# Kernel tuning notes

Measured on AMD Instinct MI355X. Metric: run time of the kernel, lower is better.

## Reference

```python
import jax, jax.numpy as jnp
import numpy as np

N, G = 10000, 200          # nodes, graphs
EL, EG = 160000, 500000    # local / global edges
S, V = 256, 64             # scalar / vector hidden dims
NA, NB = 16, 5             # atom types, bond types


def _lin(k, i, o):
    return (jax.random.normal(k, (i, o), jnp.float32) / np.sqrt(i))


def scatter_mean(vals, idx, num_segments):
    # vals: [N, ...]; idx: [N] int
    sums = jax.ops.segment_sum(vals, idx, num_segments=num_segments)
    cnt = jax.ops.segment_sum(jnp.ones((vals.shape[0],), vals.dtype), idx,
                              num_segments=num_segments)
    cnt = jnp.maximum(cnt, 1.0).reshape((-1,) + (1,) * (vals.ndim - 1))
    return sums / cnt


def calc_edge_attrs(edge_index, pos):
    src, tgt = edge_index[0], edge_index[1]
    r = pos[tgt] - pos[src]                      # [E,3]
    a = (pos[tgt] * pos[src]).sum(-1)            # [E]
    d = jnp.sqrt(jnp.clip((r ** 2).sum(-1), 1e-6))
    r_norm = r / d[:, None]
    return d, a, r_norm


def setup_inputs() -> dict:
    key = jax.random.key(0)
    ks = jax.random.split(key, 24)
    inp = {}
    inp["x"] = jax.random.normal(ks[0], (N, NA), jnp.float32)
    inp["t"] = jax.random.uniform(ks[1], (G, 1), jnp.float32)
    inp["pos"] = jax.random.normal(ks[2], (N, 3), jnp.float32)
    eil = jax.random.randint(ks[3], (2, EL), 0, N)
    eig = jax.random.randint(ks[4], (2, EG), 0, N)
    # avoid self-edges so edge distances are strictly positive (safe sqrt grads)
    eig = eig.at[1].set(jnp.where(eig[1] == eig[0], (eig[1] + 1) % N, eig[1]))
    eil = eil.at[1].set(jnp.where(eil[1] == eil[0], (eil[1] + 1) % N, eil[1]))
    inp["edge_index_local"] = eil
    inp["edge_index_global"] = eig
    inp["edge_attr_global"] = jax.random.normal(ks[5], (EG, NB), jnp.float32)
    inp["batch"] = jnp.sort(jax.random.randint(ks[6], (N,), 0, G))
    # learned parameters
    inp["W_time"], inp["b_time"] = _lin(ks[7], 1, S), jnp.zeros((S,), jnp.float32)
    inp["W_atom"], inp["b_atom"] = _lin(ks[8], NA, S), jnp.zeros((S,), jnp.float32)
    inp["W_at"], inp["b_at"] = _lin(ks[9], S, S), jnp.zeros((S,), jnp.float32)
    inp["W_shared"], inp["b_shared"] = _lin(ks[10], S, S), jnp.zeros((S,), jnp.float32)
    inp["W_b0"], inp["b_b0"] = _lin(ks[11], S + 1, S), jnp.zeros((S,), jnp.float32)
    inp["W_b1"], inp["b_b1"] = _lin(ks[12], S, 2 * NB), jnp.zeros((2 * NB,), jnp.float32)
    inp["W_coord"] = _lin(ks[13], V, 2)           # no bias
    inp["W_atoms"], inp["b_atoms"] = _lin(ks[14], S, 2 * NA), jnp.zeros((2 * NA,), jnp.float32)
    return inp


def reference(x, t, pos, edge_attr_global, W_time, b_time, W_atom, b_atom,
              W_at, b_at, W_shared, b_shared, W_b0, b_b0, W_b1, b_b1,
              W_coord, W_atoms, b_atoms,
              edge_index_local, edge_index_global, batch):
    # --- trunk: center positions, embed atoms + time ---
    pos = pos - scatter_mean(pos, batch, G)[batch]
    temb = t @ W_time + b_time                    # [G,S]
    tnode = temb[batch]                           # [N,S]
    s = x @ W_atom + b_atom
    s = (s + tnode) @ W_at + b_at                 # [N,S]
    # --- edge attrs (gather-compute pattern feeding the GNN) ---
    d_l, a_l, rn_l = calc_edge_attrs(edge_index_local, pos)
    d_g, a_g, rn_g = calc_edge_attrs(edge_index_global, pos)
    # GNN stand-in (identity on s, v, p): v initialized to zeros as in original
    v = jnp.zeros((N, 3, V), s.dtype)
    # --- prediction head ---
    s = jax.nn.silu(s @ W_shared + b_shared)
    j, i = edge_index_global[0], edge_index_global[1]
    d = jnp.sqrt(((pos[i] - pos[j]) ** 2).sum(-1, keepdims=True))  # [EG,1]
    edge = jnp.concatenate([s[i] + s[j], d], axis=-1)              # [EG,S+1]
    bonds = jax.nn.silu(edge @ W_b0 + b_b0) @ W_b1 + b_b1          # [EG,2*NB]
    bonds_pred, bonds_eps = bonds[:, :NB], bonds[:, NB:]
    coords = jnp.einsum('nkv,vo->nko', v, W_coord)                 # [N,3,2]
    coords = coords - scatter_mean(coords, batch, G)[batch]
    coords_eps0, coords_eps1 = coords[..., 0], coords[..., 1]      # [N,3]
    atoms = s @ W_atoms + b_atoms                                  # [N,2*NA]
    atoms_eps, atoms_pred = atoms[:, :NA], atoms[:, NA:]
    pos_c = pos - scatter_mean(pos, batch, G)[batch]
    coords_pred = pos_c + coords_eps1
    return (coords_pred, coords_eps0, atoms_pred, atoms_eps,
            bonds_pred, bonds_eps, d_l, rn_l, a_g, rn_g)
```

## Files before the change

kernel.cpp:

```cpp
#include <hip/hip_runtime.h>
#include <hip/hip_bf16.h>

typedef __hip_bfloat16 bf16;
typedef short bf16x8 __attribute__((ext_vector_type(8)));
typedef float f32x4 __attribute__((ext_vector_type(4)));
typedef float f32x2 __attribute__((ext_vector_type(2)));

#define N_NODES  10000
#define G_GRAPHS 200
#define EL_EDGES 160000
#define EG_EDGES 500000
#define S_DIM    256
#define APAD     264

#define BONDS_BLOCKS 15625
#define LOCAL_BLOCKS 625
#define B1ROW    280

#define WS_FLAG   0
#define WS_POSC   1024
#define WS_WD     31232
#define WS_BB1    34304
#define WS_WATOM  34560
#define WS_WTIME  38656
#define WS_BTIME  38912
#define WS_BATOM  39168
#define WS_BAT    39424
#define WS_BSH    39680
#define WS_BATOMS 39936
#define WS_T      40000
#define WS_X      40448
#define WT_AT     200448
#define WT_SH     233216
#define WT_B0     265984
#define WT_ATOMS  298752
#define WS_B1F8   302848
#define WS_H      303968
#define WS_BB0R   943968
#define WS_END_FLOATS 944224

#define CHAN(S)    ((((S) >> 6) << 6) + (((S) & 3) << 4) + (((S) & 63) >> 2))
#define CHANINV(k) ((((k) >> 6) << 6) + (((k) & 15) << 2) + (((k) >> 4) & 3))

#define O_CPRED 0
#define O_CEPS  30000
#define O_APRED 60000
#define O_AEPS  220000
#define O_BPRED 380000
#define O_BEPS  2880000
#define O_DL    5380000
#define O_RNL   5540000
#define O_AG    6020000
#define O_RNG   6520000

__device__ __forceinline__ float b2f(bf16 v) { return __bfloat162float(v); }
__device__ __forceinline__ bf16  f2b(float v) { return __float2bfloat16(v); }
__device__ __forceinline__ unsigned short bbits(float v) {
    bf16 b = f2b(v);
    return *reinterpret_cast<unsigned short*>(&b);
}
__device__ __forceinline__ float ldin(const void* p, int idx, int isf32) {
    return isf32 ? ((const float*)p)[idx] : b2f(((const bf16*)p)[idx]);
}
__device__ __forceinline__ void stout(void* out, int f32o, size_t idx, float v) {
    if (f32o) ((float*)out)[idx] = v;
    else      ((bf16*)out)[idx]  = f2b(v);
}
__device__ __forceinline__ float silu(float p) {
    return p * __builtin_amdgcn_rcpf(1.0f + __expf(-p));
}
__device__ __forceinline__ int dtype_f32(const void* tt) {
    const unsigned short* q = (const unsigned short*)tt;
    int c = 0;
#pragma unroll
    for (int z = 0; z < 32; ++z) c += (q[z] >= 0x4000) ? 1 : 0;
    return c > 0;
}

__global__ void k_prep(const void* __restrict__ x, const void* __restrict__ tt,
                       const void* __restrict__ W_time, const void* __restrict__ b_time,
                       const void* __restrict__ W_atom, const void* __restrict__ b_atom,
                       const void* __restrict__ W_at, const void* __restrict__ b_at,
                       const void* __restrict__ W_shared, const void* __restrict__ b_shared,
                       const void* __restrict__ W_b0, const void* __restrict__ b_b0,
                       const void* __restrict__ W_b1, const void* __restrict__ b_b1,
                       const void* __restrict__ W_atoms, const void* __restrict__ b_atoms,
                       float* __restrict__ ws) {
    const int t = blockIdx.x * blockDim.x + threadIdx.x;
    const int f = dtype_f32(tt);
    if (t == 0) ws[WS_FLAG] = f ? 1.0f : 0.0f;
    if (t < 65536) {
        const int k = t >> 8, n = t & 255;
        ((unsigned short*)(ws + WT_AT))[n * 256 + k] = bbits(ldin(W_at, t, f));
        ((unsigned short*)(ws + WT_SH))[n * 256 + k] = bbits(ldin(W_shared, t, f));
        ((unsigned short*)(ws + WT_B0))[n * 256 + k] = bbits(ldin(W_b0, t, f));
    }
    if (t < 160000) ws[WS_X + t] = ldin(x, t, f);
    if (t < 8192) {
        const int k = t >> 5, n = t & 31;
        ((unsigned short*)(ws + WT_ATOMS))[n * 256 + k] = bbits(ldin(W_atoms, t, f));
    }
    if (t < 4480) {
        const int n = t / B1ROW, s = t - n * B1ROW;
        float v = (n < 10 && s < 256) ? ldin(W_b1, CHAN(s) * 10 + n, f) : 0.0f;
        int enc = __builtin_amdgcn_cvt_pk_fp8_f32(v, 0.0f, 0, false);
        ((unsigned char*)(ws + WS_B1F8))[t] = (unsigned char)(enc & 0xff);
    }
    if (t < 4096) ws[WS_WATOM + t] = ldin(W_atom, t, f);
    if (t < 256) {
        ws[WS_WD + t]   = ldin(W_b0, 65536 + CHAN(t), f);
        ws[WS_BB0R + t] = ldin(b_b0, t, f);
        ws[WS_WTIME + t] = ldin(W_time, t, f);
        ws[WS_BTIME + t] = ldin(b_time, t, f);
        ws[WS_BATOM + t] = ldin(b_atom, t, f);
        ws[WS_BAT + t]   = ldin(b_at, t, f);
        ws[WS_BSH + t]   = ldin(b_shared, t, f);
    }
    if (t < 200) ws[WS_T + t] = ldin(tt, t, f);
    if (t < 32)  ws[WS_BATOMS + t] = ldin(b_atoms, t, f);
    if (t < 16)  ws[WS_BB1 + t] = (t < 10) ? ldin(b_b1, t, f) : 0.0f;
}

__global__ void k_pos(const void* __restrict__ pos, const int* __restrict__ batch,
                      float* __restrict__ ws, void* __restrict__ out) {
    const int g = blockIdx.x;
    const int f32o = ws[WS_FLAG] != 0.0f;
    __shared__ int s_lo, s_hi;
    __shared__ float wsum[4][3];
    __shared__ float mean[3];
    if (threadIdx.x == 0) {
        int lo = 0, hi = N_NODES;
        while (lo < hi) { int m = (lo + hi) >> 1; if (batch[m] < g) lo = m + 1; else hi = m; }
        s_lo = lo;
        int lo2 = lo; hi = N_NODES;
        while (lo2 < hi) { int m = (lo2 + hi) >> 1; if (batch[m] < g + 1) lo2 = m + 1; else hi = m; }
        s_hi = lo2;
    }
    __syncthreads();
    const int lo = s_lo, hi = s_hi, cnt = hi - lo;
    float sx = 0.f, sy = 0.f, sz = 0.f;
    for (int n = lo + threadIdx.x; n < hi; n += 256) {
        sx += ldin(pos, n * 3 + 0, f32o);
        sy += ldin(pos, n * 3 + 1, f32o);
        sz += ldin(pos, n * 3 + 2, f32o);
    }
#pragma unroll
    for (int off = 32; off > 0; off >>= 1) {
        sx += __shfl_down(sx, off);
        sy += __shfl_down(sy, off);
        sz += __shfl_down(sz, off);
    }
    if ((threadIdx.x & 63) == 0) {
        wsum[threadIdx.x >> 6][0] = sx;
        wsum[threadIdx.x >> 6][1] = sy;
        wsum[threadIdx.x >> 6][2] = sz;
    }
    __syncthreads();
    if (threadIdx.x == 0) {
        float inv = 1.0f / (float)max(cnt, 1);
        mean[0] = (wsum[0][0] + wsum[1][0] + wsum[2][0] + wsum[3][0]) * inv;
        mean[1] = (wsum[0][1] + wsum[1][1] + wsum[2][1] + wsum[3][1]) * inv;
        mean[2] = (wsum[0][2] + wsum[1][2] + wsum[2][2] + wsum[3][2]) * inv;
    }
    __syncthreads();
    for (int n = lo + threadIdx.x; n < hi; n += 256) {
#pragma unroll
        for (int k = 0; k < 3; ++k) {
            float p = ldin(pos, n * 3 + k, f32o) - mean[k];
            ws[WS_POSC + n * 3 + k] = p;
            stout(out, f32o, O_CPRED + n * 3 + k, p);
            stout(out, f32o, O_CEPS + n * 3 + k, 0.0f);
        }
    }
}

__global__ __launch_bounds__(256) void k_node(
    const int* __restrict__ batch, const float* __restrict__ ws,
    unsigned int* __restrict__ h_out, void* __restrict__ out) {
    __shared__ unsigned short actA[16][APAD];
    __shared__ unsigned short actB[16][APAD];
    const int tid = threadIdx.x;
    const int wave = tid >> 6, lane = tid & 63;
    const int quad = lane >> 4, l16 = lane & 15;
    const int row0 = blockIdx.x * 16;

    {
        const int r = tid >> 4;
        const int c0 = (tid & 15) * 16;
        const int g = row0 + r;
        float tb = ws[WS_T + batch[g]];
        float xr[16];
#pragma unroll
        for (int k = 0; k < 16; ++k) xr[k] = ws[WS_X + g * 16 + k];
        for (int cc = 0; cc < 16; cc += 4) {
            const int c = c0 + cc;
            float a0 = ws[WS_BATOM + c + 0] + tb * ws[WS_WTIME + c + 0] + ws[WS_BTIME + c + 0];
            float a1 = ws[WS_BATOM + c + 1] + tb * ws[WS_WTIME + c + 1] + ws[WS_BTIME + c + 1];
            float a2 = ws[WS_BATOM + c + 2] + tb * ws[WS_WTIME + c + 2] + ws[WS_BTIME + c + 2];
            float a3 = ws[WS_BATOM + c + 3] + tb * ws[WS_WTIME + c + 3] + ws[WS_BTIME + c + 3];
#pragma unroll
            for (int k = 0; k < 16; ++k) {
                float4 w4 = *(const float4*)(ws + WS_WATOM + k * S_DIM + c);
                a0 += xr[k] * w4.x; a1 += xr[k] * w4.y;
                a2 += xr[k] * w4.z; a3 += xr[k] * w4.w;
            }
            actA[r][c + 0] = bbits(a0); actA[r][c + 1] = bbits(a1);
            actA[r][c + 2] = bbits(a2); actA[r][c + 3] = bbits(a3);
        }
    }
    __syncthreads();

    const unsigned short* wt_at = (const unsigned short*)(ws + WT_AT);
    const unsigned short* wt_sh = (const unsigned short*)(ws + WT_SH);
    const unsigned short* wt_b0 = (const unsigned short*)(ws + WT_B0);
    const unsigned short* wt_am = (const unsigned short*)(ws + WT_ATOMS);
    const int n0 = wave * 64;

    {
        f32x4 acc[4] = {};
        for (int kk = 0; kk < S_DIM; kk += 32) {
            const int k = kk + quad * 8;
            bf16x8 a = *(const bf16x8*)&actA[l16][k];
#pragma unroll
            for (int nt = 0; nt < 4; ++nt) {
                bf16x8 b = *(const bf16x8*)(wt_at + (size_t)(n0 + nt * 16 + l16) * S_DIM + k);
                acc[nt] = __builtin_amdgcn_mfma_f32_16x16x32_bf16(a, b, acc[nt], 0, 0, 0);
            }
        }
#pragma unroll
        for (int nt = 0; nt < 4; ++nt) {
            const int n = n0 + nt * 16 + l16;
            const float bv = ws[WS_BAT + n];
#pragma unroll
            for (int r = 0; r < 4; ++r)
                actB[quad * 4 + r][n] = bbits(acc[nt][r] + bv);
        }
    }
    __syncthreads();

    {
        f32x4 acc[4] = {};
        for (int kk = 0; kk < S_DIM; kk += 32) {
            const int k = kk + quad * 8;
            bf16x8 a = *(const bf16x8*)&actB[l16][k];
#pragma unroll
            for (int nt = 0; nt < 4; ++nt) {
                bf16x8 b = *(const bf16x8*)(wt_sh + (size_t)(n0 + nt * 16 + l16) * S_DIM + k);
                acc[nt] = __builtin_amdgcn_mfma_f32_16x16x32_bf16(a, b, acc[nt], 0, 0, 0);
            }
        }
        __syncthreads();
#pragma unroll
        for (int nt = 0; nt < 4; ++nt) {
            const int n = n0 + nt * 16 + l16;
            const float bv = ws[WS_BSH + n];
#pragma unroll
            for (int r = 0; r < 4; ++r)
                actA[quad * 4 + r][n] = bbits(silu(acc[nt][r] + bv));
        }
    }
    __syncthreads();

    {
        f32x4 acc[4] = {};
        for (int kk = 0; kk < S_DIM; kk += 32) {
            const int k = kk + quad * 8;
            bf16x8 a = *(const bf16x8*)&actA[l16][k];
#pragma unroll
            for (int nt = 0; nt < 4; ++nt) {
                bf16x8 b = *(const bf16x8*)(wt_b0 + (size_t)(n0 + nt * 16 + l16) * S_DIM + k);
                acc[nt] = __builtin_amdgcn_mfma_f32_16x16x32_bf16(a, b, acc[nt], 0, 0, 0);
            }
        }
        float bh[4];
#pragma unroll
        for (int nt = 0; nt < 4; ++nt) bh[nt] = 0.5f * ws[WS_BB0R + n0 + nt * 16 + l16];
#pragma unroll
        for (int r = 0; r < 4; ++r) {
            const int g = row0 + quad * 4 + r;
            int w = 0;
            w = __builtin_amdgcn_cvt_pk_fp8_f32(acc[0][r] + bh[0], acc[1][r] + bh[1], w, false);
            w = __builtin_amdgcn_cvt_pk_fp8_f32(acc[2][r] + bh[2], acc[3][r] + bh[3], w, true);
            h_out[(size_t)g * 64 + wave * 16 + l16] = (unsigned int)w;
        }
    }

    if (wave < 2) {
        f32x4 acc = {};
        const int n = wave * 16 + l16;
        for (int kk = 0; kk < S_DIM; kk += 32) {
            const int k = kk + quad * 8;
            bf16x8 a = *(const bf16x8*)&actA[l16][k];
            bf16x8 b = *(const bf16x8*)(wt_am + (size_t)n * S_DIM + k);
            acc = __builtin_amdgcn_mfma_f32_16x16x32_bf16(a, b, acc, 0, 0, 0);
        }
        const float bv = ws[WS_BATOMS + n];
        const int f32o = ws[WS_FLAG] != 0.0f;
#pragma unroll
        for (int r = 0; r < 4; ++r) {
            const int g = row0 + quad * 4 + r;
            float v = acc[r] + bv;
            if (n < 16) stout(out, f32o, O_AEPS + (size_t)g * 16 + n, v);
            else        stout(out, f32o, O_APRED + (size_t)g * 16 + (n - 16), v);
        }
    }
}

__global__ __launch_bounds__(256, 7) void k_edges(const int* __restrict__ eig,
                                                  const int* __restrict__ eil,
                                                  const float* __restrict__ ws,
                                                  const unsigned char* __restrict__ h,
                                                  void* __restrict__ out) {
    __shared__ unsigned char sm[2][32][272];
    __shared__ float cwd[256];
    __shared__ long cwb1l[16 * B1ROW / 8];
    unsigned char* cwb1 = (unsigned char*)cwb1l;
    const int f32o = ws[WS_FLAG] != 0.0f;

    if (blockIdx.x >= BONDS_BLOCKS) {
        const int e = (blockIdx.x - BONDS_BLOCKS) * 256 + threadIdx.x;
        const float* posc = ws + WS_POSC;
        const int s = eil[e];
        const int t = eil[EL_EDGES + e];
        float rx = posc[t * 3 + 0] - posc[s * 3 + 0];
        float ry = posc[t * 3 + 1] - posc[s * 3 + 1];
        float rz = posc[t * 3 + 2] - posc[s * 3 + 2];
        float dsq = rx * rx + ry * ry + rz * rz;
        float d = sqrtf(fmaxf(dsq, 1e-6f));
        float inv = 1.0f / d;
        stout(out, f32o, O_DL + e, d);
        stout(out, f32o, O_RNL + (size_t)e * 3 + 0, rx * inv);
        stout(out, f32o, O_RNL + (size_t)e * 3 + 1, ry * inv);
        stout(out, f32o, O_RNL + (size_t)e * 3 + 2, rz * inv);
        return;
    }

    {
        const int t = threadIdx.x;
        cwd[t] = ws[WS_WD + t];
        const unsigned int* src = (const unsigned int*)(ws + WS_B1F8);
        unsigned int* dst = (unsigned int*)cwb1;
        for (int q = t; q < 16 * B1ROW / 4; q += 256) dst[q] = src[q];
    }

    const int wave = threadIdx.x >> 6, lane = threadIdx.x & 63;
    const int quad = lane >> 4, l16 = lane & 15;
    const int P = wave >> 1, sub = wave & 1;
    const int e0 = blockIdx.x * 32 + P * 16;

    uint4 tmp[4];
#pragma unroll
    for (int p = 0; p < 4; ++p) {
        const int r16 = p * 4 + quad;
        const int es = e0 + r16;
        const int node = sub ? eig[es] : eig[EG_EDGES + es];
        tmp[p] = *(const uint4*)(h + (size_t)node * 256 + l16 * 16);
    }
#pragma unroll
    for (int p = 0; p < 4; ++p) {
        const int row = sub * 16 + p * 4 + quad;
        *(uint4*)&sm[P][row][l16 * 16] = tmp[p];
    }

    if (sub == 0) {
        const int e = e0 + l16;
        const int j = eig[e];
        const int i = eig[EG_EDGES + e];
        const float* posc = ws + WS_POSC;
        float pix = posc[i * 3 + 0], piy = posc[i * 3 + 1], piz = posc[i * 3 + 2];
        float pjx = posc[j * 3 + 0], pjy = posc[j * 3 + 1], pjz = posc[j * 3 + 2];
        float rx = pix - pjx, ry = piy - pjy, rz = piz - pjz;
        float dsq = rx * rx + ry * ry + rz * rz;
        if (quad == 0) {
            float ag = pix * pjx + piy * pjy + piz * pjz;
            float inv = 1.0f / sqrtf(fmaxf(dsq, 1e-6f));
            stout(out, f32o, O_AG + e, ag);
            stout(out, f32o, O_RNG + (size_t)e * 3 + 0, rx * inv);
            stout(out, f32o, O_RNG + (size_t)e * 3 + 1, ry * inv);
            stout(out, f32o, O_RNG + (size_t)e * 3 + 2, rz * inv);
            *(float*)&sm[P][l16][256] = sqrtf(dsq);
        }
    }
    __syncthreads();

    const float d = *(const float*)&sm[P][l16][256];
    const unsigned char* cw = cwb1 + (size_t)l16 * B1ROW;

    const int kbase = sub * 128;
    f32x4 acc = {};
#pragma unroll
    for (int t = 0; t < 4; ++t) {
        const int k = kbase + t * 32 + quad * 8;
        uint2 uaw = *(const uint2*)&sm[P][l16][k];
        uint2 ubw = *(const uint2*)&sm[P][16 + l16][k];
        float4 wA = *(const float4*)(cwd + k);
        float4 wB = *(const float4*)(cwd + k + 4);
        f32x2 a01 = __builtin_amdgcn_cvt_pk_f32_fp8((int)uaw.x, false);
        f32x2 a23 = __builtin_amdgcn_cvt_pk_f32_fp8((int)uaw.x, true);
        f32x2 a45 = __builtin_amdgcn_cvt_pk_f32_fp8((int)uaw.y, false);
        f32x2 a67 = __builtin_amdgcn_cvt_pk_f32_fp8((int)uaw.y, true);
        f32x2 b01 = __builtin_amdgcn_cvt_pk_f32_fp8((int)ubw.x, false);
        f32x2 b23 = __builtin_amdgcn_cvt_pk_f32_fp8((int)ubw.x, true);
        f32x2 b45 = __builtin_amdgcn_cvt_pk_f32_fp8((int)ubw.y, false);
        f32x2 b67 = __builtin_amdgcn_cvt_pk_f32_fp8((int)ubw.y, true);
        float u0 = silu(fmaf(d, wA.x, a01.x + b01.x));
        float u1 = silu(fmaf(d, wA.y, a01.y + b01.y));
        float u2 = silu(fmaf(d, wA.z, a23.x + b23.x));
        float u3 = silu(fmaf(d, wA.w, a23.y + b23.y));
        float u4 = silu(fmaf(d, wB.x, a45.x + b45.x));
        float u5 = silu(fmaf(d, wB.y, a45.y + b45.y));
        float u6 = silu(fmaf(d, wB.z, a67.x + b67.x));
        float u7 = silu(fmaf(d, wB.w, a67.y + b67.y));
        int lo = __builtin_amdgcn_cvt_pk_fp8_f32(u0, u1, 0, false);
        lo = __builtin_amdgcn_cvt_pk_fp8_f32(u2, u3, lo, true);
        int hi = __builtin_amdgcn_cvt_pk_fp8_f32(u4, u5, 0, false);
        hi = __builtin_amdgcn_cvt_pk_fp8_f32(u6, u7, hi, true);
        long a64 = (long)(((unsigned long)(unsigned int)hi << 32) | (unsigned int)lo);
        long b64 = *(const long*)(cw + k);
        acc = __builtin_amdgcn_mfma_f32_16x16x32_fp8_fp8(a64, b64, acc, 0, 0, 0);
    }

    __syncthreads();
    f32x4* sc = (f32x4*)&sm[P][0][0];
    if (sub == 1) sc[lane] = acc;
    __syncthreads();
    if (sub == 0 && l16 < 10) {
        f32x4 o = sc[lane];
        const float bv = ws[WS_BB1 + l16];
#pragma unroll
        for (int r = 0; r < 4; ++r) {
            const int er = e0 + quad * 4 + r;
            float v = acc[r] + o[r] + bv;
            if (l16 < 5) stout(out, f32o, O_BPRED + (size_t)er * 5 + l16, v);
            else         stout(out, f32o, O_BEPS + (size_t)er * 5 + (l16 - 5), v);
        }
    }
}

extern "C" void kernel_launch(void* const* d_in, const int* in_sizes, int n_in,
                              void* d_out, int out_size, void* d_ws, size_t ws_size,
                              hipStream_t stream) {
    const void* x        = d_in[0];
    const void* t        = d_in[1];
    const void* pos      = d_in[2];
    const int*  eil      = (const int*)d_in[3];
    const int*  eig      = (const int*)d_in[4];
    const int*  batch    = (const int*)d_in[6];
    const void* W_time   = d_in[7];
    const void* b_time   = d_in[8];
    const void* W_atom   = d_in[9];
    const void* b_atom   = d_in[10];
    const void* W_at     = d_in[11];
    const void* b_at     = d_in[12];
    const void* W_shared = d_in[13];
    const void* b_shared = d_in[14];
    const void* W_b0     = d_in[15];
    const void* b_b0     = d_in[16];
    const void* W_b1     = d_in[17];
    const void* b_b1     = d_in[18];
    const void* W_atoms  = d_in[20];
    const void* b_atoms  = d_in[21];
    (void)in_sizes; (void)n_in; (void)out_size;

    const size_t NEED = (size_t)WS_END_FLOATS * sizeof(float);
    if (ws_size < NEED) return;

    float* ws = (float*)d_ws;
    unsigned int* hbuf = (unsigned int*)(ws + WS_H);

    k_prep<<<640, 256, 0, stream>>>(x, t, W_time, b_time, W_atom, b_atom,
                                    W_at, b_at, W_shared, b_shared, W_b0, b_b0,
                                    W_b1, b_b1, W_atoms, b_atoms, ws);
    k_pos<<<G_GRAPHS, 256, 0, stream>>>(pos, batch, ws, d_out);
    k_node<<<N_NODES / 16, 256, 0, stream>>>(batch, ws, hbuf, d_out);
    k_edges<<<BONDS_BLOCKS + LOCAL_BLOCKS, 256, 0, stream>>>(
        eig, eil, ws, (const unsigned char*)hbuf, d_out);
}
```

Before: 222.7 us.

## Process 32 node rows per block in k_node to reuse weight fragments

The node MLP kernel now handles 32 rows per block instead of 16. Each weight B-fragment loaded from global memory feeds two MFMAs, which halves weight traffic per row, and the grid drops from 625 to 313 blocks. The two activation buffers are merged into a single shared buffer, with an extra barrier added so a layer's outputs are not written while other waves are still reading its inputs. Bounds checks cover the partial last block. The node kernel is small next to the edge kernel, so any end-to-end effect is likely minor, and fewer blocks means less parallelism on this step.

```diff
diff --git a/kernel.cpp b/kernel.cpp
--- a/kernel.cpp
+++ b/kernel.cpp
@@ -13,6 +13,8 @@
 #define S_DIM    256
 #define APAD     264
 
+#define NODE_M       32
+#define NODE_BLOCKS  313
 #define BONDS_BLOCKS 15625
 #define LOCAL_BLOCKS 625
 #define B1ROW    280
@@ -177,35 +179,41 @@
 __global__ __launch_bounds__(256) void k_node(
     const int* __restrict__ batch, const float* __restrict__ ws,
     unsigned int* __restrict__ h_out, void* __restrict__ out) {
-    __shared__ unsigned short actA[16][APAD];
-    __shared__ unsigned short actB[16][APAD];
+    __shared__ unsigned short act[NODE_M][APAD];
     const int tid = threadIdx.x;
     const int wave = tid >> 6, lane = tid & 63;
     const int quad = lane >> 4, l16 = lane & 15;
-    const int row0 = blockIdx.x * 16;
+    const int row0 = blockIdx.x * NODE_M;
 
     {
-        const int r = tid >> 4;
-        const int c0 = (tid & 15) * 16;
+        const int r = tid >> 3;
+        const int c0 = (tid & 7) * 32;
         const int g = row0 + r;
-        float tb = ws[WS_T + batch[g]];
-        float xr[16];
-#pragma unroll
-        for (int k = 0; k < 16; ++k) xr[k] = ws[WS_X + g * 16 + k];
-        for (int cc = 0; cc < 16; cc += 4) {
-            const int c = c0 + cc;
-            float a0 = ws[WS_BATOM + c + 0] + tb * ws[WS_WTIME + c + 0] + ws[WS_BTIME + c + 0];
-            float a1 = ws[WS_BATOM + c + 1] + tb * ws[WS_WTIME + c + 1] + ws[WS_BTIME + c + 1];
-            float a2 = ws[WS_BATOM + c + 2] + tb * ws[WS_WTIME + c + 2] + ws[WS_BTIME + c + 2];
-            float a3 = ws[WS_BATOM + c + 3] + tb * ws[WS_WTIME + c + 3] + ws[WS_BTIME + c + 3];
-#pragma unroll
-            for (int k = 0; k < 16; ++k) {
-                float4 w4 = *(const float4*)(ws + WS_WATOM + k * S_DIM + c);
-                a0 += xr[k] * w4.x; a1 += xr[k] * w4.y;
-                a2 += xr[k] * w4.z; a3 += xr[k] * w4.w;
-            }
-            actA[r][c + 0] = bbits(a0); actA[r][c + 1] = bbits(a1);
-            actA[r][c + 2] = bbits(a2); actA[r][c + 3] = bbits(a3);
+        if (g < N_NODES) {
+            float tb = ws[WS_T + batch[g]];
+            float xr[16];
+#pragma unroll
+            for (int k = 0; k < 16; ++k) xr[k] = ws[WS_X + g * 16 + k];
+            for (int cc = 0; cc < 32; cc += 4) {
+                const int c = c0 + cc;
+                float a0 = ws[WS_BATOM + c + 0] + tb * ws[WS_WTIME + c + 0] + ws[WS_BTIME + c + 0];
+                float a1 = ws[WS_BATOM + c + 1] + tb * ws[WS_WTIME + c + 1] + ws[WS_BTIME + c + 1];
+                float a2 = ws[WS_BATOM + c + 2] + tb * ws[WS_WTIME + c + 2] + ws[WS_BTIME + c + 2];
+                float a3 = ws[WS_BATOM + c + 3] + tb * ws[WS_WTIME + c + 3] + ws[WS_BTIME + c + 3];
+#pragma unroll
+                for (int k = 0; k < 16; ++k) {
+                    float4 w4 = *(const float4*)(ws + WS_WATOM + k * S_DIM + c);
+                    a0 += xr[k] * w4.x; a1 += xr[k] * w4.y;
+                    a2 += xr[k] * w4.z; a3 += xr[k] * w4.w;
+                }
+                act[r][c + 0] = bbits(a0); act[r][c + 1] = bbits(a1);
+                act[r][c + 2] = bbits(a2); act[r][c + 3] = bbits(a3);
+            }
+        } else {
+            for (int cc = 0; cc < 32; cc += 4) {
+                const int c = c0 + cc;
+                act[r][c] = 0; act[r][c + 1] = 0; act[r][c + 2] = 0; act[r][c + 3] = 0;
+            }
         }
     }
     __syncthreads();
@@ -217,36 +225,43 @@
     const int n0 = wave * 64;
 
     {
-        f32x4 acc[4] = {};
+        f32x4 acc[2][4] = {};
         for (int kk = 0; kk < S_DIM; kk += 32) {
             const int k = kk + quad * 8;
-            bf16x8 a = *(const bf16x8*)&actA[l16][k];
+            bf16x8 a0 = *(const bf16x8*)&act[l16][k];
+            bf16x8 a1 = *(const bf16x8*)&act[16 + l16][k];
 #pragma unroll
             for (int nt = 0; nt < 4; ++nt) {
                 bf16x8 b = *(const bf16x8*)(wt_at + (size_t)(n0 + nt * 16 + l16) * S_DIM + k);
-                acc[nt] = __builtin_amdgcn_mfma_f32_16x16x32_bf16(a, b, acc[nt], 0, 0, 0);
-            }
-        }
+                acc[0][nt] = __builtin_amdgcn_mfma_f32_16x16x32_bf16(a0, b, acc[0][nt], 0, 0, 0);
+                acc[1][nt] = __builtin_amdgcn_mfma_f32_16x16x32_bf16(a1, b, acc[1][nt], 0, 0, 0);
+            }
+        }
+        __syncthreads();
 #pragma unroll
         for (int nt = 0; nt < 4; ++nt) {
             const int n = n0 + nt * 16 + l16;
             const float bv = ws[WS_BAT + n];
 #pragma unroll
-            for (int r = 0; r < 4; ++r)
-                actB[quad * 4 + r][n] = bbits(acc[nt][r] + bv);
+            for (int mt = 0; mt < 2; ++mt)
+#pragma unroll
+                for (int r = 0; r < 4; ++r)
+                    act[mt * 16 + quad * 4 + r][n] = bbits(acc[mt][nt][r] + bv);
         }
     }
     __syncthreads();
 
     {
-        f32x4 acc[4] = {};
+        f32x4 acc[2][4] = {};
         for (int kk = 0; kk < S_DIM; kk += 32) {
             const int k = kk + quad * 8;
-            bf16x8 a = *(const bf16x8*)&actB[l16][k];
+            bf16x8 a0 = *(const bf16x8*)&act[l16][k];
+            bf16x8 a1 = *(const bf16x8*)&act[16 + l16][k];
 #pragma unroll
             for (int nt = 0; nt < 4; ++nt) {
                 bf16x8 b = *(const bf16x8*)(wt_sh + (size_t)(n0 + nt * 16 + l16) * S_DIM + k);
-                acc[nt] = __builtin_amdgcn_mfma_f32_16x16x32_bf16(a, b, acc[nt], 0, 0, 0);
+                acc[0][nt] = __builtin_amdgcn_mfma_f32_16x16x32_bf16(a0, b, acc[0][nt], 0, 0, 0);
+                acc[1][nt] = __builtin_amdgcn_mfma_f32_16x16x32_bf16(a1, b, acc[1][nt], 0, 0, 0);
             }
         }
         __syncthreads();
@@ -255,42 +270,51 @@
             const int n = n0 + nt * 16 + l16;
             const float bv = ws[WS_BSH + n];
 #pragma unroll
-            for (int r = 0; r < 4; ++r)
-                actA[quad * 4 + r][n] = bbits(silu(acc[nt][r] + bv));
+            for (int mt = 0; mt < 2; ++mt)
+#pragma unroll
+                for (int r = 0; r < 4; ++r)
+                    act[mt * 16 + quad * 4 + r][n] = bbits(silu(acc[mt][nt][r] + bv));
         }
     }
     __syncthreads();
 
     {
-        f32x4 acc[4] = {};
+        f32x4 acc[2][4] = {};
         for (int kk = 0; kk < S_DIM; kk += 32) {
             const int k = kk + quad * 8;
-            bf16x8 a = *(const bf16x8*)&actA[l16][k];
+            bf16x8 a0 = *(const bf16x8*)&act[l16][k];
+            bf16x8 a1 = *(const bf16x8*)&act[16 + l16][k];
 #pragma unroll
             for (int nt = 0; nt < 4; ++nt) {
                 bf16x8 b = *(const bf16x8*)(wt_b0 + (size_t)(n0 + nt * 16 + l16) * S_DIM + k);
-                acc[nt] = __builtin_amdgcn_mfma_f32_16x16x32_bf16(a, b, acc[nt], 0, 0, 0);
+                acc[0][nt] = __builtin_amdgcn_mfma_f32_16x16x32_bf16(a0, b, acc[0][nt], 0, 0, 0);
+                acc[1][nt] = __builtin_amdgcn_mfma_f32_16x16x32_bf16(a1, b, acc[1][nt], 0, 0, 0);
             }
         }
         float bh[4];
 #pragma unroll
         for (int nt = 0; nt < 4; ++nt) bh[nt] = 0.5f * ws[WS_BB0R + n0 + nt * 16 + l16];
 #pragma unroll
-        for (int r = 0; r < 4; ++r) {
-            const int g = row0 + quad * 4 + r;
-            int w = 0;
-            w = __builtin_amdgcn_cvt_pk_fp8_f32(acc[0][r] + bh[0], acc[1][r] + bh[1], w, false);
-            w = __builtin_amdgcn_cvt_pk_fp8_f32(acc[2][r] + bh[2], acc[3][r] + bh[3], w, true);
-            h_out[(size_t)g * 64 + wave * 16 + l16] = (unsigned int)w;
-        }
-    }
-
-    if (wave < 2) {
+        for (int mt = 0; mt < 2; ++mt)
+#pragma unroll
+            for (int r = 0; r < 4; ++r) {
+                const int g = row0 + mt * 16 + quad * 4 + r;
+                if (g < N_NODES) {
+                    int w = 0;
+                    w = __builtin_amdgcn_cvt_pk_fp8_f32(acc[mt][0][r] + bh[0], acc[mt][1][r] + bh[1], w, false);
+                    w = __builtin_amdgcn_cvt_pk_fp8_f32(acc[mt][2][r] + bh[2], acc[mt][3][r] + bh[3], w, true);
+                    h_out[(size_t)g * 64 + wave * 16 + l16] = (unsigned int)w;
+                }
+            }
+    }
+
+    {
         f32x4 acc = {};
-        const int n = wave * 16 + l16;
+        const int mt = wave >> 1;
+        const int n = (wave & 1) * 16 + l16;
         for (int kk = 0; kk < S_DIM; kk += 32) {
             const int k = kk + quad * 8;
-            bf16x8 a = *(const bf16x8*)&actA[l16][k];
+            bf16x8 a = *(const bf16x8*)&act[mt * 16 + l16][k];
             bf16x8 b = *(const bf16x8*)(wt_am + (size_t)n * S_DIM + k);
             acc = __builtin_amdgcn_mfma_f32_16x16x32_bf16(a, b, acc, 0, 0, 0);
         }
@@ -298,10 +322,12 @@
         const int f32o = ws[WS_FLAG] != 0.0f;
 #pragma unroll
         for (int r = 0; r < 4; ++r) {
-            const int g = row0 + quad * 4 + r;
-            float v = acc[r] + bv;
-            if (n < 16) stout(out, f32o, O_AEPS + (size_t)g * 16 + n, v);
-            else        stout(out, f32o, O_APRED + (size_t)g * 16 + (n - 16), v);
+            const int g = row0 + mt * 16 + quad * 4 + r;
+            if (g < N_NODES) {
+                float v = acc[r] + bv;
+                if (n < 16) stout(out, f32o, O_AEPS + (size_t)g * 16 + n, v);
+                else        stout(out, f32o, O_APRED + (size_t)g * 16 + (n - 16), v);
+            }
         }
     }
 }
@@ -472,7 +498,7 @@
                                     W_at, b_at, W_shared, b_shared, W_b0, b_b0,
                                     W_b1, b_b1, W_atoms, b_atoms, ws);
     k_pos<<<G_GRAPHS, 256, 0, stream>>>(pos, batch, ws, d_out);
-    k_node<<<N_NODES / 16, 256, 0, stream>>>(batch, ws, hbuf, d_out);
+    k_node<<<NODE_BLOCKS, 256, 0, stream>>>(batch, ws, hbuf, d_out);
     k_edges<<<BONDS_BLOCKS + LOCAL_BLOCKS, 256, 0, stream>>>(
         eig, eil, ws, (const unsigned char*)hbuf, d_out);
 }
```

After: 234.3 us. +5.2%, slower.

## Fold atom, W_at and shared linear layers into one matrix; merge prep kernels

Applied to the files above, without the earlier changes.

With no nonlinearity between them, the atom embedding, time embedding, W_at and W_shared layers are algebraically folded into a single 16x256 matrix plus a time vector and bias. One dedicated block of a merged pre-kernel computes this fold in fp32. The per-node kernel then does a small 16-wide product followed by silu, dropping two 256x256 MFMA GEMMs per node tile and the conversion of those weights. The old prep and pos-centering kernels become one launch, and x is read directly instead of being copied. The cost is a serial single-block fold, whose latency may sit on the critical path before the node kernel starts.

```diff
diff --git a/kernel.cpp b/kernel.cpp
--- a/kernel.cpp
+++ b/kernel.cpp
@@ -13,34 +13,33 @@
 #define S_DIM    256
 #define APAD     264
 
+#define NODE_BLOCKS  625
 #define BONDS_BLOCKS 15625
 #define LOCAL_BLOCKS 625
 #define B1ROW    280
 
+#define PRE_CONV 256
+#define PRE_FOLD 256
+#define PRE_POS  257
+#define PRE_BLOCKS 457
+
 #define WS_FLAG   0
 #define WS_POSC   1024
 #define WS_WD     31232
-#define WS_BB1    34304
-#define WS_WATOM  34560
-#define WS_WTIME  38656
-#define WS_BTIME  38912
-#define WS_BATOM  39168
-#define WS_BAT    39424
-#define WS_BSH    39680
-#define WS_BATOMS 39936
-#define WS_T      40000
-#define WS_X      40448
-#define WT_AT     200448
-#define WT_SH     233216
-#define WT_B0     265984
-#define WT_ATOMS  298752
-#define WS_B1F8   302848
-#define WS_H      303968
-#define WS_BB0R   943968
-#define WS_END_FLOATS 944224
+#define WS_BB1    31744
+#define WS_WX     31760
+#define WS_WT2    35856
+#define WS_B2     36112
+#define WS_BATOMS 36368
+#define WS_T      36400
+#define WS_BB0R   36608
+#define WT_B0     36864
+#define WT_ATOMS  69632
+#define WS_B1F8   73728
+#define WS_H      74848
+#define WS_END_FLOATS 714848
 
 #define CHAN(S)    ((((S) >> 6) << 6) + (((S) & 3) << 4) + (((S) & 63) >> 2))
-#define CHANINV(k) ((((k) >> 6) << 6) + (((k) & 15) << 2) + (((k) >> 4) & 3))
 
 #define O_CPRED 0
 #define O_CEPS  30000
@@ -77,108 +76,132 @@
     return c > 0;
 }
 
-__global__ void k_prep(const void* __restrict__ x, const void* __restrict__ tt,
-                       const void* __restrict__ W_time, const void* __restrict__ b_time,
-                       const void* __restrict__ W_atom, const void* __restrict__ b_atom,
-                       const void* __restrict__ W_at, const void* __restrict__ b_at,
-                       const void* __restrict__ W_shared, const void* __restrict__ b_shared,
-                       const void* __restrict__ W_b0, const void* __restrict__ b_b0,
-                       const void* __restrict__ W_b1, const void* __restrict__ b_b1,
-                       const void* __restrict__ W_atoms, const void* __restrict__ b_atoms,
-                       float* __restrict__ ws) {
-    const int t = blockIdx.x * blockDim.x + threadIdx.x;
-    const int f = dtype_f32(tt);
-    if (t == 0) ws[WS_FLAG] = f ? 1.0f : 0.0f;
-    if (t < 65536) {
-        const int k = t >> 8, n = t & 255;
-        ((unsigned short*)(ws + WT_AT))[n * 256 + k] = bbits(ldin(W_at, t, f));
-        ((unsigned short*)(ws + WT_SH))[n * 256 + k] = bbits(ldin(W_shared, t, f));
-        ((unsigned short*)(ws + WT_B0))[n * 256 + k] = bbits(ldin(W_b0, t, f));
-    }
-    if (t < 160000) ws[WS_X + t] = ldin(x, t, f);
-    if (t < 8192) {
-        const int k = t >> 5, n = t & 31;
-        ((unsigned short*)(ws + WT_ATOMS))[n * 256 + k] = bbits(ldin(W_atoms, t, f));
-    }
-    if (t < 4480) {
-        const int n = t / B1ROW, s = t - n * B1ROW;
-        float v = (n < 10 && s < 256) ? ldin(W_b1, CHAN(s) * 10 + n, f) : 0.0f;
-        int enc = __builtin_amdgcn_cvt_pk_fp8_f32(v, 0.0f, 0, false);
-        ((unsigned char*)(ws + WS_B1F8))[t] = (unsigned char)(enc & 0xff);
-    }
-    if (t < 4096) ws[WS_WATOM + t] = ldin(W_atom, t, f);
-    if (t < 256) {
-        ws[WS_WD + t]   = ldin(W_b0, 65536 + CHAN(t), f);
-        ws[WS_BB0R + t] = ldin(b_b0, t, f);
-        ws[WS_WTIME + t] = ldin(W_time, t, f);
-        ws[WS_BTIME + t] = ldin(b_time, t, f);
-        ws[WS_BATOM + t] = ldin(b_atom, t, f);
-        ws[WS_BAT + t]   = ldin(b_at, t, f);
-        ws[WS_BSH + t]   = ldin(b_shared, t, f);
-    }
-    if (t < 200) ws[WS_T + t] = ldin(tt, t, f);
-    if (t < 32)  ws[WS_BATOMS + t] = ldin(b_atoms, t, f);
-    if (t < 16)  ws[WS_BB1 + t] = (t < 10) ? ldin(b_b1, t, f) : 0.0f;
-}
-
-__global__ void k_pos(const void* __restrict__ pos, const int* __restrict__ batch,
+__global__ void k_pre(const void* __restrict__ tt, const void* __restrict__ pos,
+                      const int* __restrict__ batch,
+                      const void* __restrict__ W_time, const void* __restrict__ b_time,
+                      const void* __restrict__ W_atom, const void* __restrict__ b_atom,
+                      const void* __restrict__ W_at, const void* __restrict__ b_at,
+                      const void* __restrict__ W_shared, const void* __restrict__ b_shared,
+                      const void* __restrict__ W_b0, const void* __restrict__ b_b0,
+                      const void* __restrict__ W_b1, const void* __restrict__ b_b1,
+                      const void* __restrict__ W_atoms, const void* __restrict__ b_atoms,
                       float* __restrict__ ws, void* __restrict__ out) {
-    const int g = blockIdx.x;
-    const int f32o = ws[WS_FLAG] != 0.0f;
+    __shared__ float T1s[18][256];
+    __shared__ int s_f;
     __shared__ int s_lo, s_hi;
     __shared__ float wsum[4][3];
     __shared__ float mean[3];
-    if (threadIdx.x == 0) {
-        int lo = 0, hi = N_NODES;
-        while (lo < hi) { int m = (lo + hi) >> 1; if (batch[m] < g) lo = m + 1; else hi = m; }
-        s_lo = lo;
-        int lo2 = lo; hi = N_NODES;
-        while (lo2 < hi) { int m = (lo2 + hi) >> 1; if (batch[m] < g + 1) lo2 = m + 1; else hi = m; }
-        s_hi = lo2;
-    }
+    if (threadIdx.x == 0) s_f = dtype_f32(tt);
     __syncthreads();
-    const int lo = s_lo, hi = s_hi, cnt = hi - lo;
-    float sx = 0.f, sy = 0.f, sz = 0.f;
-    for (int n = lo + threadIdx.x; n < hi; n += 256) {
-        sx += ldin(pos, n * 3 + 0, f32o);
-        sy += ldin(pos, n * 3 + 1, f32o);
-        sz += ldin(pos, n * 3 + 2, f32o);
-    }
-#pragma unroll
-    for (int off = 32; off > 0; off >>= 1) {
-        sx += __shfl_down(sx, off);
-        sy += __shfl_down(sy, off);
-        sz += __shfl_down(sz, off);
-    }
-    if ((threadIdx.x & 63) == 0) {
-        wsum[threadIdx.x >> 6][0] = sx;
-        wsum[threadIdx.x >> 6][1] = sy;
-        wsum[threadIdx.x >> 6][2] = sz;
-    }
-    __syncthreads();
-    if (threadIdx.x == 0) {
-        float inv = 1.0f / (float)max(cnt, 1);
-        mean[0] = (wsum[0][0] + wsum[1][0] + wsum[2][0] + wsum[3][0]) * inv;
-        mean[1] = (wsum[0][1] + wsum[1][1] + wsum[2][1] + wsum[3][1]) * inv;
-        mean[2] = (wsum[0][2] + wsum[1][2] + wsum[2][2] + wsum[3][2]) * inv;
-    }
-    __syncthreads();
-    for (int n = lo + threadIdx.x; n < hi; n += 256) {
-#pragma unroll
-        for (int k = 0; k < 3; ++k) {
-            float p = ldin(pos, n * 3 + k, f32o) - mean[k];
-            ws[WS_POSC + n * 3 + k] = p;
-            stout(out, f32o, O_CPRED + n * 3 + k, p);
-            stout(out, f32o, O_CEPS + n * 3 + k, 0.0f);
+    const int f = s_f;
+    const int b = blockIdx.x;
+
+    if (b < PRE_CONV) {
+        const int t = b * 256 + threadIdx.x;
+        if (t == 0) ws[WS_FLAG] = f ? 1.0f : 0.0f;
+        {
+            const int k = t >> 8, n = t & 255;
+            ((unsigned short*)(ws + WT_B0))[n * 256 + k] = bbits(ldin(W_b0, t, f));
+        }
+        if (t < 8192) {
+            const int k = t >> 5, n = t & 31;
+            ((unsigned short*)(ws + WT_ATOMS))[n * 256 + k] = bbits(ldin(W_atoms, t, f));
+        }
+        if (t < 4480) {
+            const int n = t / B1ROW, s = t - n * B1ROW;
+            float v = (n < 10 && s < 256) ? ldin(W_b1, CHAN(s) * 10 + n, f) : 0.0f;
+            int enc = __builtin_amdgcn_cvt_pk_fp8_f32(v, 0.0f, 0, false);
+            ((unsigned char*)(ws + WS_B1F8))[t] = (unsigned char)(enc & 0xff);
+        }
+        if (t < 256) {
+            ws[WS_WD + t]   = ldin(W_b0, 65536 + CHAN(t), f);
+            ws[WS_BB0R + t] = ldin(b_b0, t, f);
+        }
+        if (t < 200) ws[WS_T + t] = ldin(tt, t, f);
+        if (t < 32)  ws[WS_BATOMS + t] = ldin(b_atoms, t, f);
+        if (t < 16)  ws[WS_BB1 + t] = (t < 10) ? ldin(b_b1, t, f) : 0.0f;
+    } else if (b == PRE_FOLD) {
+        const int c = threadIdx.x;
+        float acc[18];
+#pragma unroll
+        for (int r = 0; r < 18; ++r) acc[r] = 0.0f;
+        for (int n = 0; n < 256; ++n) {
+            const float w = ldin(W_at, n * 256 + c, f);
+#pragma unroll
+            for (int r = 0; r < 16; ++r) acc[r] += ldin(W_atom, r * 256 + n, f) * w;
+            acc[16] += (ldin(b_atom, n, f) + ldin(b_time, n, f)) * w;
+            acc[17] += ldin(W_time, n, f) * w;
+        }
+        acc[16] += ldin(b_at, c, f);
+#pragma unroll
+        for (int r = 0; r < 18; ++r) T1s[r][c] = acc[r];
+        __syncthreads();
+        float a2[18];
+#pragma unroll
+        for (int r = 0; r < 18; ++r) a2[r] = 0.0f;
+        for (int n = 0; n < 256; ++n) {
+            const float w = ldin(W_shared, n * 256 + c, f);
+#pragma unroll
+            for (int r = 0; r < 18; ++r) a2[r] += T1s[r][n] * w;
+        }
+#pragma unroll
+        for (int k = 0; k < 16; ++k) ws[WS_WX + k * 256 + c] = a2[k];
+        ws[WS_B2 + c]  = a2[16] + ldin(b_shared, c, f);
+        ws[WS_WT2 + c] = a2[17];
+    } else {
+        const int g = b - PRE_POS;
+        if (threadIdx.x == 0) {
+            int lo = 0, hi = N_NODES;
+            while (lo < hi) { int m = (lo + hi) >> 1; if (batch[m] < g) lo = m + 1; else hi = m; }
+            s_lo = lo;
+            int lo2 = lo; hi = N_NODES;
+            while (lo2 < hi) { int m = (lo2 + hi) >> 1; if (batch[m] < g + 1) lo2 = m + 1; else hi = m; }
+            s_hi = lo2;
+        }
+        __syncthreads();
+        const int lo = s_lo, hi = s_hi, cnt = hi - lo;
+        float sx = 0.f, sy = 0.f, sz = 0.f;
+        for (int n = lo + threadIdx.x; n < hi; n += 256) {
+            sx += ldin(pos, n * 3 + 0, f);
+            sy += ldin(pos, n * 3 + 1, f);
+            sz += ldin(pos, n * 3 + 2, f);
+        }
+#pragma unroll
+        for (int off = 32; off > 0; off >>= 1) {
+            sx += __shfl_down(sx, off);
+            sy += __shfl_down(sy, off);
+            sz += __shfl_down(sz, off);
+        }
+        if ((threadIdx.x & 63) == 0) {
+            wsum[threadIdx.x >> 6][0] = sx;
+            wsum[threadIdx.x >> 6][1] = sy;
+            wsum[threadIdx.x >> 6][2] = sz;
+        }
+        __syncthreads();
+        if (threadIdx.x == 0) {
+            float inv = 1.0f / (float)max(cnt, 1);
+            mean[0] = (wsum[0][0] + wsum[1][0] + wsum[2][0] + wsum[3][0]) * inv;
+            mean[1] = (wsum[0][1] + wsum[1][1] + wsum[2][1] + wsum[3][1]) * inv;
+            mean[2] = (wsum[0][2] + wsum[1][2] + wsum[2][2] + wsum[3][2]) * inv;
+        }
+        __syncthreads();
+        for (int n = lo + threadIdx.x; n < hi; n += 256) {
+#pragma unroll
+            for (int k = 0; k < 3; ++k) {
+                float p = ldin(pos, n * 3 + k, f) - mean[k];
+                ws[WS_POSC + n * 3 + k] = p;
+                stout(out, f, O_CPRED + n * 3 + k, p);
+                stout(out, f, O_CEPS + n * 3 + k, 0.0f);
+            }
         }
     }
 }
 
 __global__ __launch_bounds__(256) void k_node(
-    const int* __restrict__ batch, const float* __restrict__ ws,
-    unsigned int* __restrict__ h_out, void* __restrict__ out) {
-    __shared__ unsigned short actA[16][APAD];
-    __shared__ unsigned short actB[16][APAD];
+    const void* __restrict__ x, const int* __restrict__ batch,
+    const float* __restrict__ ws, unsigned int* __restrict__ h_out,
+    void* __restrict__ out) {
+    __shared__ unsigned short act[16][APAD];
     const int tid = threadIdx.x;
     const int wave = tid >> 6, lane = tid & 63;
     const int quad = lane >> 4, l16 = lane & 15;
@@ -188,30 +211,29 @@
         const int r = tid >> 4;
         const int c0 = (tid & 15) * 16;
         const int g = row0 + r;
-        float tb = ws[WS_T + batch[g]];
+        const int f32o = ws[WS_FLAG] != 0.0f;
+        const float tb = ws[WS_T + batch[g]];
         float xr[16];
 #pragma unroll
-        for (int k = 0; k < 16; ++k) xr[k] = ws[WS_X + g * 16 + k];
+        for (int k = 0; k < 16; ++k) xr[k] = ldin(x, g * 16 + k, f32o);
         for (int cc = 0; cc < 16; cc += 4) {
             const int c = c0 + cc;
-            float a0 = ws[WS_BATOM + c + 0] + tb * ws[WS_WTIME + c + 0] + ws[WS_BTIME + c + 0];
-            float a1 = ws[WS_BATOM + c + 1] + tb * ws[WS_WTIME + c + 1] + ws[WS_BTIME + c + 1];
-            float a2 = ws[WS_BATOM + c + 2] + tb * ws[WS_WTIME + c + 2] + ws[WS_BTIME + c + 2];
-            float a3 = ws[WS_BATOM + c + 3] + tb * ws[WS_WTIME + c + 3] + ws[WS_BTIME + c + 3];
+            float a0 = ws[WS_B2 + c + 0] + tb * ws[WS_WT2 + c + 0];
+            float a1 = ws[WS_B2 + c + 1] + tb * ws[WS_WT2 + c + 1];
+            float a2 = ws[WS_B2 + c + 2] + tb * ws[WS_WT2 + c + 2];
+            float a3 = ws[WS_B2 + c + 3] + tb * ws[WS_WT2 + c + 3];
 #pragma unroll
             for (int k = 0; k < 16; ++k) {
-                float4 w4 = *(const float4*)(ws + WS_WATOM + k * S_DIM + c);
+                float4 w4 = *(const float4*)(ws + WS_WX + k * S_DIM + c);
                 a0 += xr[k] * w4.x; a1 += xr[k] * w4.y;
                 a2 += xr[k] * w4.z; a3 += xr[k] * w4.w;
             }
-            actA[r][c + 0] = bbits(a0); actA[r][c + 1] = bbits(a1);
-            actA[r][c + 2] = bbits(a2); actA[r][c + 3] = bbits(a3);
+            act[r][c + 0] = bbits(silu(a0)); act[r][c + 1] = bbits(silu(a1));
+            act[r][c + 2] = bbits(silu(a2)); act[r][c + 3] = bbits(silu(a3));
         }
     }
     __syncthreads();
 
-    const unsigned short* wt_at = (const unsigned short*)(ws + WT_AT);
-    const unsigned short* wt_sh = (const unsigned short*)(ws + WT_SH);
     const unsigned short* wt_b0 = (const unsigned short*)(ws + WT_B0);
     const unsigned short* wt_am = (const unsigned short*)(ws + WT_ATOMS);
     const int n0 = wave * 64;
@@ -220,52 +242,7 @@
         f32x4 acc[4] = {};
         for (int kk = 0; kk < S_DIM; kk += 32) {
             const int k = kk + quad * 8;
-            bf16x8 a = *(const bf16x8*)&actA[l16][k];
-#pragma unroll
-            for (int nt = 0; nt < 4; ++nt) {
-                bf16x8 b = *(const bf16x8*)(wt_at + (size_t)(n0 + nt * 16 + l16) * S_DIM + k);
-                acc[nt] = __builtin_amdgcn_mfma_f32_16x16x32_bf16(a, b, acc[nt], 0, 0, 0);
-            }
-        }
-#pragma unroll
-        for (int nt = 0; nt < 4; ++nt) {
-            const int n = n0 + nt * 16 + l16;
-            const float bv = ws[WS_BAT + n];
-#pragma unroll
-            for (int r = 0; r < 4; ++r)
-                actB[quad * 4 + r][n] = bbits(acc[nt][r] + bv);
-        }
-    }
-    __syncthreads();
-
-    {
-        f32x4 acc[4] = {};
-        for (int kk = 0; kk < S_DIM; kk += 32) {
-            const int k = kk + quad * 8;
-            bf16x8 a = *(const bf16x8*)&actB[l16][k];
-#pragma unroll
-            for (int nt = 0; nt < 4; ++nt) {
-                bf16x8 b = *(const bf16x8*)(wt_sh + (size_t)(n0 + nt * 16 + l16) * S_DIM + k);
-                acc[nt] = __builtin_amdgcn_mfma_f32_16x16x32_bf16(a, b, acc[nt], 0, 0, 0);
-            }
-        }
-        __syncthreads();
-#pragma unroll
-        for (int nt = 0; nt < 4; ++nt) {
-            const int n = n0 + nt * 16 + l16;
-            const float bv = ws[WS_BSH + n];
-#pragma unroll
-            for (int r = 0; r < 4; ++r)
-                actA[quad * 4 + r][n] = bbits(silu(acc[nt][r] + bv));
-        }
-    }
-    __syncthreads();
-
-    {
-        f32x4 acc[4] = {};
-        for (int kk = 0; kk < S_DIM; kk += 32) {
-            const int k = kk + quad * 8;
-            bf16x8 a = *(const bf16x8*)&actA[l16][k];
+            bf16x8 a = *(const bf16x8*)&act[l16][k];
 #pragma unroll
             for (int nt = 0; nt < 4; ++nt) {
                 bf16x8 b = *(const bf16x8*)(wt_b0 + (size_t)(n0 + nt * 16 + l16) * S_DIM + k);
@@ -290,7 +267,7 @@
         const int n = wave * 16 + l16;
         for (int kk = 0; kk < S_DIM; kk += 32) {
             const int k = kk + quad * 8;
-            bf16x8 a = *(const bf16x8*)&actA[l16][k];
+            bf16x8 a = *(const bf16x8*)&act[l16][k];
             bf16x8 b = *(const bf16x8*)(wt_am + (size_t)n * S_DIM + k);
             acc = __builtin_amdgcn_mfma_f32_16x16x32_bf16(a, b, acc, 0, 0, 0);
         }
@@ -468,11 +445,11 @@
     float* ws = (float*)d_ws;
     unsigned int* hbuf = (unsigned int*)(ws + WS_H);
 
-    k_prep<<<640, 256, 0, stream>>>(x, t, W_time, b_time, W_atom, b_atom,
-                                    W_at, b_at, W_shared, b_shared, W_b0, b_b0,
-                                    W_b1, b_b1, W_atoms, b_atoms, ws);
-    k_pos<<<G_GRAPHS, 256, 0, stream>>>(pos, batch, ws, d_out);
-    k_node<<<N_NODES / 16, 256, 0, stream>>>(batch, ws, hbuf, d_out);
+    k_pre<<<PRE_BLOCKS, 256, 0, stream>>>(t, pos, batch, W_time, b_time, W_atom,
+                                          b_atom, W_at, b_at, W_shared, b_shared,
+                                          W_b0, b_b0, W_b1, b_b1, W_atoms, b_atoms,
+                                          ws, d_out);
+    k_node<<<NODE_BLOCKS, 256, 0, stream>>>(x, batch, ws, hbuf, d_out);
     k_edges<<<BONDS_BLOCKS + LOCAL_BLOCKS, 256, 0, stream>>>(
         eig, eil, ws, (const unsigned char*)hbuf, d_out);
 }
```

Measured after the change: 524.2 us. 2.35x slower.
